# Optimization experiments

Hardware: AMD Instinct MI355X
Metric: run time of the kernel (lower is better)

## Reference

```python
import jax, jax.numpy as jnp
import numpy as np

N, L, D = 64, 510, 768
L1, K, OUT = 128, 20, 300
EPS = 1e-5


def _make_spans(key, n, n_spans, max_len):
    ks, kl = jax.random.split(key)
    starts = jnp.sort(jax.random.randint(ks, (n, n_spans), 0, max_len - 4), axis=1)
    lens = jax.random.randint(kl, (n, n_spans), 1, 5)
    ends = jnp.minimum(starts + lens, max_len)
    return starts.astype(jnp.int32), ends.astype(jnp.int32)


def setup_inputs() -> dict:
    key = jax.random.key(0)
    ks = jax.random.split(key, 10)
    t1 = jax.random.normal(ks[0], (N, L, D), jnp.float32)
    encoded_know = jax.random.normal(ks[1], (N, L, D), jnp.float32)
    span_starts, span_ends = _make_spans(ks[2], N, L1, L)
    know_span_starts, know_span_ends = _make_spans(ks[3], N, K, L)
    # padding masks: True = masked; guarantee >=1 valid entry per row
    valid1 = jax.random.randint(ks[4], (N,), L1 // 2, L1 + 1)
    key_padding_mask = jnp.arange(L1)[None, :] >= valid1[:, None]
    validk = jax.random.randint(ks[5], (N,), 5, K + 1)
    key_padding_mask_know = jnp.arange(K)[None, :] >= validk[:, None]
    W_lin = jax.random.normal(ks[6], (OUT, D), jnp.float32) * 0.02
    b_lin = jnp.zeros((OUT,), jnp.float32)
    gamma = jnp.ones((OUT,), jnp.float32)
    beta = jnp.zeros((OUT,), jnp.float32)
    W_score = jax.random.normal(ks[7], (1, OUT), jnp.float32) * 0.02
    b_score = jnp.zeros((1,), jnp.float32)
    return dict(t1=t1, encoded_know=encoded_know,
                span_starts=span_starts, span_ends=span_ends,
                key_padding_mask=key_padding_mask,
                know_span_starts=know_span_starts, know_span_ends=know_span_ends,
                key_padding_mask_know=key_padding_mask_know,
                W_lin=W_lin, b_lin=b_lin, gamma=gamma, beta=beta,
                W_score=W_score, b_score=b_score)


def _span_mean(x, starts, ends):
    # x: (N,L,D); spans [s,e) -> mean via inclusive-scan difference (one pass)
    n, l, d = x.shape
    cs = jnp.concatenate([jnp.zeros((n, 1, d), x.dtype), jnp.cumsum(x, axis=1)], axis=1)
    gather = lambda idx: jnp.take_along_axis(cs, idx[:, :, None].astype(jnp.int32), axis=1)
    sums = gather(ends) - gather(starts)  # (N, n_spans, D)
    lens = jnp.maximum(ends - starts, 1).astype(x.dtype)[:, :, None]
    return sums / lens


def _layernorm(x, g, b):
    m = jnp.mean(x, axis=-1, keepdims=True)
    v = jnp.mean(jnp.square(x - m), axis=-1, keepdims=True)
    return (x - m) * jax.lax.rsqrt(v + EPS) * g + b


def reference(t1, encoded_know, span_starts, span_ends, key_padding_mask,
              know_span_starts, know_span_ends, key_padding_mask_know,
              W_lin, b_lin, gamma, beta, W_score, b_score):
    lam = 1.0

    def branch(x, s, e, mask):
        pooled = _span_mean(x, s, e)                       # ragged segment mean
        h = _layernorm(pooled @ W_lin.T + b_lin, gamma, beta)
        sc = (h @ W_score.T + b_score)[..., 0]             # (N, n_spans)
        sc = jnp.where(mask, -jnp.inf, sc)                 # masked_fill
        return h, jax.nn.softmax(sc * lam, axis=1)

    h1, s1 = branch(t1, span_starts, span_ends, key_padding_mask)
    hk, sk = branch(encoded_know, know_span_starts, know_span_ends, key_padding_mask_know)
    score = jnp.broadcast_to(s1[:, :, None], h1.shape)     # repeat to (N,L1,OUT)
    return h1, score, hk, sk
```

## Files before the change

kernel.cpp:

```cpp
#include <hip/hip_runtime.h>
#include <hip/hip_bf16.h>
#include <stdint.h>

#define NB    64
#define LSEQ  510
#define DIN   768
#define L1S   128
#define KS    20
#define OUTF  300
#define NPAD  320
#define EPSL  1e-5f

#define M1    (NB * L1S)
#define MK    (NB * KS)
#define MT    (M1 + MK)

#define OFF_H1    0
#define OFF_SCORE (M1 * OUTF)
#define OFF_HK    (2 * M1 * OUTF)
#define OFF_SK    (OFF_HK + MK * OUTF)

#define WS_FLAG    0
#define WS_SCORES  64
#define WS_PROBS   40960
#define WS_WBF     81920
#define WS_POOLED  589824

typedef short  short8_t  __attribute__((ext_vector_type(8)));
typedef float  float4v_t __attribute__((ext_vector_type(4)));
typedef unsigned short ushort4_t __attribute__((ext_vector_type(4)));

__global__ void detect_mask_kernel(const unsigned int* __restrict__ p, int* flag) {
    __shared__ int f_bf16, f_f32, f_other;
    if (threadIdx.x == 0) { f_bf16 = 0; f_f32 = 0; f_other = 0; }
    __syncthreads();
    for (int i = threadIdx.x; i < 2048; i += blockDim.x) {
        unsigned int v = p[i];
        if (v <= 1u) continue;
        if (v == 0x3F803F80u)       atomicOr(&f_bf16, 1);
        else if (v == 0x3F800000u)  atomicOr(&f_f32, 1);
        else                        atomicOr(&f_other, 1);
    }
    __syncthreads();
    if (threadIdx.x == 0) {
        int f = 0;
        if (f_bf16)       f = 3;
        else if (f_f32)   f = 2;
        else if (f_other) f = 1;
        *flag = f;
    }
}

__device__ inline bool mask_at(const void* m, int idx, int flag) {
    switch (flag) {
        case 1:  return ((const unsigned char*)m)[idx] != 0;
        case 2:  return ((const float*)m)[idx] != 0.0f;
        case 3:  return ((const unsigned short*)m)[idx] != 0;
        default: return ((const int*)m)[idx] != 0;
    }
}

__global__ __launch_bounds__(256)
void wconv_kernel(const float* __restrict__ W, unsigned short* __restrict__ Wb) {
    int idx = blockIdx.x * 256 + threadIdx.x;
    if (idx >= NPAD * DIN) return;
    int r = idx / DIN;
    float v = (r < OUTF) ? W[idx - (r - (r < OUTF ? 0 : 0)) * 0 + 0] : 0.f;
    int c = idx - r * DIN;
    v = (r < OUTF) ? W[(size_t)r * DIN + c] : 0.f;
    __hip_bfloat16 b = __float2bfloat16(v);
    Wb[idx] = *(unsigned short*)&b;
}

__global__ __launch_bounds__(256)
void pool_kernel(const float* __restrict__ t1,
                 const float* __restrict__ know,
                 const int* __restrict__ s1s, const int* __restrict__ s1e,
                 const int* __restrict__ kss, const int* __restrict__ kse,
                 unsigned short* __restrict__ pooled) {
    const int wave = threadIdx.x >> 6;
    const int lane = threadIdx.x & 63;
    const int g = blockIdx.x * 4 + wave;
    const float* x;
    int n, s, e;
    if (g < M1) {
        n = g >> 7;
        x = t1;  s = s1s[g]; e = s1e[g];
    } else {
        int gg = g - M1;
        n = gg / KS;
        x = know; s = kss[gg]; e = kse[gg];
    }
    if (s < 0) s = 0;
    if (e > LSEQ) e = LSEQ;
    int len = e - s; if (len < 1) len = 1;
    const float inv = 1.0f / (float)len;
    const float4* base = (const float4*)(x + (size_t)n * LSEQ * DIN);

    unsigned short* orow = pooled + (size_t)g * DIN;
#pragma unroll
    for (int j = 0; j < 3; ++j) {
        int c4 = lane + j * 64;
        float4 acc = make_float4(0.f, 0.f, 0.f, 0.f);
        for (int r = s; r < e; ++r) {
            float4 v = base[(size_t)r * (DIN / 4) + c4];
            acc.x += v.x; acc.y += v.y; acc.z += v.z; acc.w += v.w;
        }
        __hip_bfloat16 b0 = __float2bfloat16(acc.x * inv);
        __hip_bfloat16 b1 = __float2bfloat16(acc.y * inv);
        __hip_bfloat16 b2 = __float2bfloat16(acc.z * inv);
        __hip_bfloat16 b3 = __float2bfloat16(acc.w * inv);
        ushort4_t pk;
        pk.x = *(unsigned short*)&b0; pk.y = *(unsigned short*)&b1;
        pk.z = *(unsigned short*)&b2; pk.w = *(unsigned short*)&b3;
        *(ushort4_t*)(orow + c4 * 4) = pk;
    }
}

__global__ __launch_bounds__(320)
void gemm_mfma_kernel(const unsigned short* __restrict__ Apool,
                      const unsigned short* __restrict__ Wb,
                      const float* __restrict__ bias,
                      const float* __restrict__ gamma,
                      const float* __restrict__ beta,
                      const float* __restrict__ Wsc,
                      const float* __restrict__ bsc,
                      float* __restrict__ out,
                      float* __restrict__ scores) {
    __shared__ float sC[16][NPAD + 1];

    const int tid  = threadIdx.x;
    const int wave = tid >> 6;
    const int lane = tid & 63;
    const int quad = lane >> 4;
    const int l16  = lane & 15;
    const int R0   = blockIdx.x * 16;

    const unsigned short* arow = Apool + (size_t)(R0 + l16) * DIN + quad * 8;
    const unsigned short* brow0 = Wb + (size_t)(wave * 64 + 0 * 16 + l16) * DIN + quad * 8;
    const unsigned short* brow1 = Wb + (size_t)(wave * 64 + 1 * 16 + l16) * DIN + quad * 8;
    const unsigned short* brow2 = Wb + (size_t)(wave * 64 + 2 * 16 + l16) * DIN + quad * 8;
    const unsigned short* brow3 = Wb + (size_t)(wave * 64 + 3 * 16 + l16) * DIN + quad * 8;

    float4v_t acc0 = {0.f, 0.f, 0.f, 0.f};
    float4v_t acc1 = {0.f, 0.f, 0.f, 0.f};
    float4v_t acc2 = {0.f, 0.f, 0.f, 0.f};
    float4v_t acc3 = {0.f, 0.f, 0.f, 0.f};

#pragma unroll 4
    for (int k0 = 0; k0 < DIN; k0 += 32) {
        short8_t a  = *(const short8_t*)(arow + k0);
        short8_t b0 = *(const short8_t*)(brow0 + k0);
        short8_t b1 = *(const short8_t*)(brow1 + k0);
        short8_t b2 = *(const short8_t*)(brow2 + k0);
        short8_t b3 = *(const short8_t*)(brow3 + k0);
        acc0 = __builtin_amdgcn_mfma_f32_16x16x32_bf16(a, b0, acc0, 0, 0, 0);
        acc1 = __builtin_amdgcn_mfma_f32_16x16x32_bf16(a, b1, acc1, 0, 0, 0);
        acc2 = __builtin_amdgcn_mfma_f32_16x16x32_bf16(a, b2, acc2, 0, 0, 0);
        acc3 = __builtin_amdgcn_mfma_f32_16x16x32_bf16(a, b3, acc3, 0, 0, 0);
    }

#pragma unroll
    for (int i = 0; i < 4; ++i) {
        sC[quad * 4 + i][wave * 64 +  0 + l16] = acc0[i];
        sC[quad * 4 + i][wave * 64 + 16 + l16] = acc1[i];
        sC[quad * 4 + i][wave * 64 + 32 + l16] = acc2[i];
        sC[quad * 4 + i][wave * 64 + 48 + l16] = acc3[i];
    }
    __syncthreads();

    if (wave < 4) {
        const float bs0 = bsc[0];
#pragma unroll
        for (int rr = 0; rr < 4; ++rr) {
            const int r = wave * 4 + rr;
            const int g = R0 + r;
            float s = 0.f;
            float tv[5];
#pragma unroll
            for (int m = 0; m < 5; ++m) {
                int c = lane + 64 * m;
                float v = (c < OUTF) ? (sC[r][c] + bias[c]) : 0.f;
                tv[m] = v; s += v;
            }
#pragma unroll
            for (int off = 32; off > 0; off >>= 1) s += __shfl_xor(s, off, 64);
            const float mean = s * (1.0f / OUTF);
            float vs = 0.f;
#pragma unroll
            for (int m = 0; m < 5; ++m) {
                int c = lane + 64 * m;
                float d = (c < OUTF) ? (tv[m] - mean) : 0.f;
                vs += d * d;
            }
#pragma unroll
            for (int off = 32; off > 0; off >>= 1) vs += __shfl_xor(vs, off, 64);
            const float rstd = rsqrtf(vs * (1.0f / OUTF) + EPSL);
            const size_t off0 = (g < M1) ? (size_t)OFF_H1 + (size_t)g * OUTF
                                         : (size_t)OFF_HK + (size_t)(g - M1) * OUTF;
            float sc = 0.f;
#pragma unroll
            for (int m = 0; m < 5; ++m) {
                int c = lane + 64 * m;
                if (c < OUTF) {
                    float h = (tv[m] - mean) * rstd * gamma[c] + beta[c];
                    out[off0 + c] = h;
                    sc += h * Wsc[c];
                }
            }
#pragma unroll
            for (int off = 32; off > 0; off >>= 1) sc += __shfl_xor(sc, off, 64);
            if (lane == 0) scores[g] = sc + bs0;
        }
    }
}

__global__ __launch_bounds__(256)
void softmax_kernel(const float* __restrict__ scores,
                    const void* __restrict__ m1,
                    const void* __restrict__ mk,
                    const int* __restrict__ flagp,
                    float* __restrict__ probs,
                    float* __restrict__ out) {
    const int flag = *flagp;
    const int w = blockIdx.x * 4 + (threadIdx.x >> 6);
    const int lane = threadIdx.x & 63;

    if (w < NB) {
        const int n = w;
        float v0 = scores[n * L1S + lane];
        float v1 = scores[n * L1S + lane + 64];
        if (mask_at(m1, n * L1S + lane, flag))      v0 = -INFINITY;
        if (mask_at(m1, n * L1S + lane + 64, flag)) v1 = -INFINITY;
        float mx = fmaxf(v0, v1);
#pragma unroll
        for (int off = 32; off > 0; off >>= 1) mx = fmaxf(mx, __shfl_xor(mx, off, 64));
        float e0 = __expf(v0 - mx);
        float e1 = __expf(v1 - mx);
        float s = e0 + e1;
#pragma unroll
        for (int off = 32; off > 0; off >>= 1) s += __shfl_xor(s, off, 64);
        float inv = 1.0f / s;
        probs[n * L1S + lane]      = e0 * inv;
        probs[n * L1S + lane + 64] = e1 * inv;
    } else {
        const int n = w - NB;
        float v = -INFINITY;
        if (lane < KS) {
            v = scores[M1 + n * KS + lane];
            if (mask_at(mk, n * KS + lane, flag)) v = -INFINITY;
        }
        float mx = v;
#pragma unroll
        for (int off = 32; off > 0; off >>= 1) mx = fmaxf(mx, __shfl_xor(mx, off, 64));
        float e = (lane < KS) ? __expf(v - mx) : 0.f;
        float s = e;
#pragma unroll
        for (int off = 32; off > 0; off >>= 1) s += __shfl_xor(s, off, 64);
        if (lane < KS) out[(size_t)OFF_SK + n * KS + lane] = e / s;
    }
}

__global__ __launch_bounds__(256)
void bcast_kernel(const float* __restrict__ probs, float* __restrict__ out) {
    const int e0 = (blockIdx.x * 256 + threadIdx.x) * 4;
    float4 v;
    v.x = probs[(e0 + 0) / OUTF];
    v.y = probs[(e0 + 1) / OUTF];
    v.z = probs[(e0 + 2) / OUTF];
    v.w = probs[(e0 + 3) / OUTF];
    *(float4*)(out + (size_t)OFF_SCORE + e0) = v;
}

extern "C" void kernel_launch(void* const* d_in, const int* in_sizes, int n_in,
                              void* d_out, int out_size, void* d_ws, size_t ws_size,
                              hipStream_t stream) {
    const float* t1   = (const float*)d_in[0];
    const float* know = (const float*)d_in[1];
    const int* s1s = (const int*)d_in[2];
    const int* s1e = (const int*)d_in[3];
    const void* m1 = d_in[4];
    const int* kss = (const int*)d_in[5];
    const int* kse = (const int*)d_in[6];
    const void* mk = d_in[7];
    const float* Wl  = (const float*)d_in[8];
    const float* bl  = (const float*)d_in[9];
    const float* gm  = (const float*)d_in[10];
    const float* bt  = (const float*)d_in[11];
    const float* Wsc = (const float*)d_in[12];
    const float* bsc = (const float*)d_in[13];
    float* out = (float*)d_out;

    char* ws = (char*)d_ws;
    int*            flag   = (int*)(ws + WS_FLAG);
    float*          scores = (float*)(ws + WS_SCORES);
    float*          probs  = (float*)(ws + WS_PROBS);
    unsigned short* Wb     = (unsigned short*)(ws + WS_WBF);
    unsigned short* pooled = (unsigned short*)(ws + WS_POOLED);

    detect_mask_kernel<<<1, 256, 0, stream>>>((const unsigned int*)m1, flag);
    wconv_kernel<<<(NPAD * DIN + 255) / 256, 256, 0, stream>>>(Wl, Wb);
    pool_kernel<<<MT / 4, 256, 0, stream>>>(t1, know, s1s, s1e, kss, kse, pooled);
    gemm_mfma_kernel<<<MT / 16, 320, 0, stream>>>(pooled, Wb, bl, gm, bt, Wsc, bsc,
                                                  out, scores);
    softmax_kernel<<<32, 256, 0, stream>>>(scores, m1, mk, flag, probs, out);
    bcast_kernel<<<(M1 * OUTF) / 1024, 256, 0, stream>>>(probs, out);
}
```

Before: 282.1 us.

## Fuse span pooling into MFMA GEMM kernel with split-K across waves

Result: faster. 267.0 us (-5.4%).

```diff
diff --git a/kernel.cpp b/kernel.cpp
--- a/kernel.cpp
+++ b/kernel.cpp
@@ -24,11 +24,14 @@
 #define WS_SCORES  64
 #define WS_PROBS   40960
 #define WS_WBF     81920
-#define WS_POOLED  589824
 
 typedef short  short8_t  __attribute__((ext_vector_type(8)));
 typedef float  float4v_t __attribute__((ext_vector_type(4)));
 typedef unsigned short ushort4_t __attribute__((ext_vector_type(4)));
+
+#define SA_STRIDE 776
+#define SC_STRIDE 324
+#define LDS_BYTES 41984
 
 __global__ void detect_mask_kernel(const unsigned int* __restrict__ p, int* flag) {
     __shared__ int f_bf16, f_f32, f_other;
@@ -65,47 +68,60 @@
     int idx = blockIdx.x * 256 + threadIdx.x;
     if (idx >= NPAD * DIN) return;
     int r = idx / DIN;
-    float v = (r < OUTF) ? W[idx - (r - (r < OUTF ? 0 : 0)) * 0 + 0] : 0.f;
-    int c = idx - r * DIN;
-    v = (r < OUTF) ? W[(size_t)r * DIN + c] : 0.f;
+    float v = (r < OUTF) ? W[idx] : 0.f;
     __hip_bfloat16 b = __float2bfloat16(v);
     Wb[idx] = *(unsigned short*)&b;
 }
 
-__global__ __launch_bounds__(256)
-void pool_kernel(const float* __restrict__ t1,
-                 const float* __restrict__ know,
-                 const int* __restrict__ s1s, const int* __restrict__ s1e,
-                 const int* __restrict__ kss, const int* __restrict__ kse,
-                 unsigned short* __restrict__ pooled) {
-    const int wave = threadIdx.x >> 6;
-    const int lane = threadIdx.x & 63;
-    const int g = blockIdx.x * 4 + wave;
-    const float* x;
-    int n, s, e;
-    if (g < M1) {
-        n = g >> 7;
-        x = t1;  s = s1s[g]; e = s1e[g];
-    } else {
-        int gg = g - M1;
-        n = gg / KS;
-        x = know; s = kss[gg]; e = kse[gg];
-    }
-    if (s < 0) s = 0;
-    if (e > LSEQ) e = LSEQ;
-    int len = e - s; if (len < 1) len = 1;
-    const float inv = 1.0f / (float)len;
-    const float4* base = (const float4*)(x + (size_t)n * LSEQ * DIN);
-
-    unsigned short* orow = pooled + (size_t)g * DIN;
-#pragma unroll
-    for (int j = 0; j < 3; ++j) {
-        int c4 = lane + j * 64;
-        float4 acc = make_float4(0.f, 0.f, 0.f, 0.f);
-        for (int r = s; r < e; ++r) {
-            float4 v = base[(size_t)r * (DIN / 4) + c4];
+__global__ __launch_bounds__(640, 5)
+void fused_gemm_kernel(const float* __restrict__ t1,
+                       const float* __restrict__ know,
+                       const int* __restrict__ s1s, const int* __restrict__ s1e,
+                       const int* __restrict__ kss, const int* __restrict__ kse,
+                       const unsigned short* __restrict__ Wb,
+                       const float* __restrict__ bias,
+                       const float* __restrict__ gamma,
+                       const float* __restrict__ beta,
+                       const float* __restrict__ Wsc,
+                       const float* __restrict__ bsc,
+                       float* __restrict__ out,
+                       float* __restrict__ scores) {
+    __shared__ unsigned long long lds_raw[LDS_BYTES / 8];
+    unsigned short* sA   = (unsigned short*)lds_raw;
+    int*   sSrc = (int*)  ((char*)lds_raw + 16 * 1552);
+    int*   sLen = (int*)  ((char*)lds_raw + 16 * 1552 + 64);
+    float* sInv = (float*)((char*)lds_raw + 16 * 1552 + 128);
+
+    const int tid = threadIdx.x;
+    const int R0  = blockIdx.x * 16;
+    const bool isk = (R0 >= M1);
+
+    if (tid < 16) {
+        int g = R0 + tid;
+        int s, e, n;
+        if (!isk) { n = g >> 7;          s = s1s[g];      e = s1e[g]; }
+        else      { int gg = g - M1; n = gg / KS; s = kss[gg]; e = kse[gg]; }
+        if (s < 0) s = 0;
+        if (e > LSEQ) e = LSEQ;
+        int len = e - s; if (len < 1) len = 1;
+        sSrc[tid] = n * (LSEQ * (DIN / 4)) + s * (DIN / 4);
+        sLen[tid] = len;
+        sInv[tid] = 1.0f / (float)len;
+    }
+    __syncthreads();
+
+    const float4* src4 = (const float4*)(isk ? know : t1);
+    for (int t = tid; t < 16 * 192; t += 640) {
+        int sp = t / 192;
+        int c4 = t - sp * 192;
+        const float4* p = src4 + sSrc[sp] + c4;
+        int len = sLen[sp];
+        float4 acc = p[0];
+        for (int r = 1; r < len; ++r) {
+            float4 v = p[r * 192];
             acc.x += v.x; acc.y += v.y; acc.z += v.z; acc.w += v.w;
         }
+        float inv = sInv[sp];
         __hip_bfloat16 b0 = __float2bfloat16(acc.x * inv);
         __hip_bfloat16 b1 = __float2bfloat16(acc.y * inv);
         __hip_bfloat16 b2 = __float2bfloat16(acc.z * inv);
@@ -113,34 +129,19 @@
         ushort4_t pk;
         pk.x = *(unsigned short*)&b0; pk.y = *(unsigned short*)&b1;
         pk.z = *(unsigned short*)&b2; pk.w = *(unsigned short*)&b3;
-        *(ushort4_t*)(orow + c4 * 4) = pk;
-    }
-}
-
-__global__ __launch_bounds__(320)
-void gemm_mfma_kernel(const unsigned short* __restrict__ Apool,
-                      const unsigned short* __restrict__ Wb,
-                      const float* __restrict__ bias,
-                      const float* __restrict__ gamma,
-                      const float* __restrict__ beta,
-                      const float* __restrict__ Wsc,
-                      const float* __restrict__ bsc,
-                      float* __restrict__ out,
-                      float* __restrict__ scores) {
-    __shared__ float sC[16][NPAD + 1];
-
-    const int tid  = threadIdx.x;
+        *(ushort4_t*)(sA + sp * SA_STRIDE + c4 * 4) = pk;
+    }
+    __syncthreads();
+
     const int wave = tid >> 6;
     const int lane = tid & 63;
     const int quad = lane >> 4;
     const int l16  = lane & 15;
-    const int R0   = blockIdx.x * 16;
-
-    const unsigned short* arow = Apool + (size_t)(R0 + l16) * DIN + quad * 8;
-    const unsigned short* brow0 = Wb + (size_t)(wave * 64 + 0 * 16 + l16) * DIN + quad * 8;
-    const unsigned short* brow1 = Wb + (size_t)(wave * 64 + 1 * 16 + l16) * DIN + quad * 8;
-    const unsigned short* brow2 = Wb + (size_t)(wave * 64 + 2 * 16 + l16) * DIN + quad * 8;
-    const unsigned short* brow3 = Wb + (size_t)(wave * 64 + 3 * 16 + l16) * DIN + quad * 8;
+    const int cg   = wave % 5;
+    const int kh   = wave / 5;
+
+    const unsigned short* sArow = sA + l16 * SA_STRIDE + quad * 8 + kh * 384;
+    const unsigned short* bb = Wb + (size_t)(cg * 64 + l16) * DIN + quad * 8 + kh * 384;
 
     float4v_t acc0 = {0.f, 0.f, 0.f, 0.f};
     float4v_t acc1 = {0.f, 0.f, 0.f, 0.f};
@@ -148,39 +149,44 @@
     float4v_t acc3 = {0.f, 0.f, 0.f, 0.f};
 
 #pragma unroll 4
-    for (int k0 = 0; k0 < DIN; k0 += 32) {
-        short8_t a  = *(const short8_t*)(arow + k0);
-        short8_t b0 = *(const short8_t*)(brow0 + k0);
-        short8_t b1 = *(const short8_t*)(brow1 + k0);
-        short8_t b2 = *(const short8_t*)(brow2 + k0);
-        short8_t b3 = *(const short8_t*)(brow3 + k0);
+    for (int k0 = 0; k0 < 384; k0 += 32) {
+        short8_t a  = *(const short8_t*)(sArow + k0);
+        short8_t b0 = *(const short8_t*)(bb + 0 * 16 * DIN + k0);
+        short8_t b1 = *(const short8_t*)(bb + 1 * 16 * DIN + k0);
+        short8_t b2 = *(const short8_t*)(bb + 2 * 16 * DIN + k0);
+        short8_t b3 = *(const short8_t*)(bb + 3 * 16 * DIN + k0);
         acc0 = __builtin_amdgcn_mfma_f32_16x16x32_bf16(a, b0, acc0, 0, 0, 0);
         acc1 = __builtin_amdgcn_mfma_f32_16x16x32_bf16(a, b1, acc1, 0, 0, 0);
         acc2 = __builtin_amdgcn_mfma_f32_16x16x32_bf16(a, b2, acc2, 0, 0, 0);
         acc3 = __builtin_amdgcn_mfma_f32_16x16x32_bf16(a, b3, acc3, 0, 0, 0);
     }
 
+    __syncthreads();
+    float* sC = (float*)lds_raw;
 #pragma unroll
     for (int i = 0; i < 4; ++i) {
-        sC[quad * 4 + i][wave * 64 +  0 + l16] = acc0[i];
-        sC[quad * 4 + i][wave * 64 + 16 + l16] = acc1[i];
-        sC[quad * 4 + i][wave * 64 + 32 + l16] = acc2[i];
-        sC[quad * 4 + i][wave * 64 + 48 + l16] = acc3[i];
-    }
-    __syncthreads();
-
-    if (wave < 4) {
+        int r = (kh * 16 + quad * 4 + i) * SC_STRIDE + cg * 64 + l16;
+        sC[r +  0] = acc0[i];
+        sC[r + 16] = acc1[i];
+        sC[r + 32] = acc2[i];
+        sC[r + 48] = acc3[i];
+    }
+    __syncthreads();
+
+    if (wave < 8) {
         const float bs0 = bsc[0];
 #pragma unroll
-        for (int rr = 0; rr < 4; ++rr) {
-            const int r = wave * 4 + rr;
+        for (int rr = 0; rr < 2; ++rr) {
+            const int r = wave * 2 + rr;
             const int g = R0 + r;
+            float tv[5];
             float s = 0.f;
-            float tv[5];
 #pragma unroll
             for (int m = 0; m < 5; ++m) {
                 int c = lane + 64 * m;
-                float v = (c < OUTF) ? (sC[r][c] + bias[c]) : 0.f;
+                float v = 0.f;
+                if (c < OUTF)
+                    v = sC[r * SC_STRIDE + c] + sC[(16 + r) * SC_STRIDE + c] + bias[c];
                 tv[m] = v; s += v;
             }
 #pragma unroll
@@ -196,8 +202,9 @@
 #pragma unroll
             for (int off = 32; off > 0; off >>= 1) vs += __shfl_xor(vs, off, 64);
             const float rstd = rsqrtf(vs * (1.0f / OUTF) + EPSL);
-            const size_t off0 = (g < M1) ? (size_t)OFF_H1 + (size_t)g * OUTF
-                                         : (size_t)OFF_HK + (size_t)(g - M1) * OUTF;
+
+            const size_t off0 = isk ? (size_t)OFF_HK + (size_t)(g - M1) * OUTF
+                                    : (size_t)g * OUTF;
             float sc = 0.f;
 #pragma unroll
             for (int m = 0; m < 5; ++m) {
@@ -296,13 +303,12 @@
     float*          scores = (float*)(ws + WS_SCORES);
     float*          probs  = (float*)(ws + WS_PROBS);
     unsigned short* Wb     = (unsigned short*)(ws + WS_WBF);
-    unsigned short* pooled = (unsigned short*)(ws + WS_POOLED);
 
     detect_mask_kernel<<<1, 256, 0, stream>>>((const unsigned int*)m1, flag);
     wconv_kernel<<<(NPAD * DIN + 255) / 256, 256, 0, stream>>>(Wl, Wb);
-    pool_kernel<<<MT / 4, 256, 0, stream>>>(t1, know, s1s, s1e, kss, kse, pooled);
-    gemm_mfma_kernel<<<MT / 16, 320, 0, stream>>>(pooled, Wb, bl, gm, bt, Wsc, bsc,
-                                                  out, scores);
+    fused_gemm_kernel<<<MT / 16, 640, 0, stream>>>(t1, know, s1s, s1e, kss, kse,
+                                                   Wb, bl, gm, bt, Wsc, bsc,
+                                                   out, scores);
     softmax_kernel<<<32, 256, 0, stream>>>(scores, m1, mk, flag, probs, out);
     bcast_kernel<<<(M1 * OUTF) / 1024, 256, 0, stream>>>(probs, out);
 }
```
